# Optimization experiments

Hardware: AMD Instinct MI355X
Metric: run time of the kernel (lower is better)

The kernel has to match this reference:

```python
import jax, jax.numpy as jnp
import numpy as np
import math

B, S, H = 2, 2048, 2048
NH, HD = 16, 128           # num_heads, head_dim; num_kv_heads == num_heads (MHA)
THETA = 10000.0


def setup_inputs() -> dict:
    key = jax.random.key(0)
    ks = jax.random.split(key, 5)
    scale = 0.02
    hidden_states = jax.random.normal(ks[0], (B, S, H), jnp.float32)
    q_w = jax.random.normal(ks[1], (H, H), jnp.float32) * scale
    k_w = jax.random.normal(ks[2], (H, H), jnp.float32) * scale
    v_w = jax.random.normal(ks[3], (H, H), jnp.float32) * scale
    o_w = jax.random.normal(ks[4], (H, H), jnp.float32) * scale
    # additive causal mask, finite large-negative (as HF builds it)
    causal = jnp.tril(jnp.ones((S, S), bool))
    attention_mask = jnp.where(causal, 0.0, -1e9).astype(jnp.float32)[None, None]  # [1,1,S,S]
    position_ids = jnp.broadcast_to(jnp.arange(S, dtype=jnp.int64), (B, S))
    return {
        "hidden_states": hidden_states,
        "q_w": q_w, "k_w": k_w, "v_w": v_w, "o_w": o_w,
        "attention_mask": attention_mask,
        "position_ids": position_ids,
    }


def _rotate_half(x):
    x1, x2 = x[..., : x.shape[-1] // 2], x[..., x.shape[-1] // 2 :]
    return jnp.concatenate((-x2, x1), axis=-1)


def _rope_cos_sin(position_ids):
    inv_freq = 1.0 / (THETA ** (jnp.arange(0, HD, 2, dtype=jnp.float32) / HD))  # [HD/2]
    freqs = position_ids.astype(jnp.float32)[:, :, None] * inv_freq[None, None, :]  # [B,S,HD/2]
    emb = jnp.concatenate((freqs, freqs), axis=-1)  # [B,S,HD]
    # unsqueeze head dim (unsqueeze_dim=1 after transpose to [B,H,S,D])
    return jnp.cos(emb)[:, None], jnp.sin(emb)[:, None]  # [B,1,S,HD]


def reference(hidden_states, q_w, k_w, v_w, o_w, attention_mask, position_ids):
    # projections (torch Linear: y = x @ W^T), split heads -> [B,NH,S,HD]
    def proj(w):
        return jnp.einsum('bsh,oh->bso', hidden_states, w).reshape(B, S, NH, HD).transpose(0, 2, 1, 3)
    q, k, v = proj(q_w), proj(k_w), proj(v_w)

    cos, sin = _rope_cos_sin(position_ids)
    q = q * cos + _rotate_half(q) * sin
    k = k * cos + _rotate_half(k) * sin

    scores = jnp.einsum('bhqd,bhkd->bhqk', q, k) / math.sqrt(HD)  # [B,NH,S,S]
    scores = scores + attention_mask
    attn = jax.nn.softmax(scores, axis=-1)  # dropout p=0.0 -> identity
    out = jnp.einsum('bhqk,bhkd->bhqd', attn, v)  # [B,NH,S,HD]
    out = out.transpose(0, 2, 1, 3).reshape(B, S, H)
    return jnp.einsum('bsh,oh->bso', out, o_w)
```

## Files before the change

kernel.cpp:

```cpp
#include <hip/hip_runtime.h>
#include <hip/hip_bf16.h>

using bf16 = __hip_bfloat16;
typedef short  short8  __attribute__((ext_vector_type(8)));
typedef float  float4_ __attribute__((ext_vector_type(4)));
typedef int    int4_   __attribute__((ext_vector_type(4)));

typedef __attribute__((address_space(1))) const void* gas_ptr;
typedef __attribute__((address_space(3))) void*       las_ptr;

#define MFMA_BF16(a, b, c) __builtin_amdgcn_mfma_f32_16x16x32_bf16((a), (b), (c), 0, 0, 0)

__device__ __forceinline__ float bf2f(bf16 v) { return __bfloat162float(v); }
__device__ __forceinline__ bf16  f2bf(float v) { return __float2bfloat16(v); }

#define BAR() do { asm volatile("" ::: "memory"); __builtin_amdgcn_s_barrier(); asm volatile("" ::: "memory"); } while (0)
#define WAITLGKM0() asm volatile("s_waitcnt lgkmcnt(0)" ::: "memory")

__global__ __launch_bounds__(256)
void cvt_all(const float* __restrict__ X,  const float* __restrict__ Wq,
             const float* __restrict__ Wk, const float* __restrict__ Wv,
             const float* __restrict__ Wo,
             bf16* __restrict__ Xb,  bf16* __restrict__ Wqb,
             bf16* __restrict__ Wkb, bf16* __restrict__ Wvb,
             bf16* __restrict__ Wob)
{
    const size_t i = ((size_t)blockIdx.x * 256 + threadIdx.x) * 8;
    const float* src; bf16* dst; size_t off;
    if (i < 8388608)       { src = X;  dst = Xb;  off = i; }
    else if (i < 12582912) { src = Wq; dst = Wqb; off = i - 8388608; }
    else if (i < 16777216) { src = Wk; dst = Wkb; off = i - 12582912; }
    else if (i < 20971520) { src = Wv; dst = Wvb; off = i - 16777216; }
    else                   { src = Wo; dst = Wob; off = i - 20971520; }
    const float4_ a = *(const float4_*)(src + off);
    const float4_ b = *(const float4_*)(src + off + 4);
    union { short8 s; bf16 h[8]; } u;
#pragma unroll
    for (int j = 0; j < 4; ++j) { u.h[j] = f2bf(a[j]); u.h[j + 4] = f2bf(b[j]); }
    *(short8*)(dst + off) = u.s;
}

__global__ __launch_bounds__(512, 2)
void gemm_bn128(const bf16* __restrict__ Ap, const bf16* __restrict__ Wp,
                bf16* __restrict__ Oq, float* __restrict__ OF, int mode)
{
    constexpr int NT = 32;
    __shared__ bf16 As0[2 * 256 * 64];
    __shared__ bf16 Bs0[2 * 128 * 64];

    const int nwg  = gridDim.x * gridDim.y;
    const int bid0 = blockIdx.y * gridDim.x + blockIdx.x;
    const int cpx  = nwg >> 3;
    const int swzb = (bid0 & 7) * cpx + (bid0 >> 3);
    const int bn = (swzb % gridDim.x) * 128;
    const int bm = (swzb / gridDim.x) * 256;

    const int tid  = threadIdx.x;
    const int w    = tid >> 6;
    const int ln   = tid & 63;
    const int r15  = ln & 15;
    const int quad = ln >> 4;
    const int wr   = w >> 1;
    const int wc   = w & 1;

    const int srow = ln >> 3;
    const int scol = ((ln & 7) ^ srow) * 8;
    const int w8   = w * 8;
    const int cx   = (r15 & 7) * 8;

#define STAGE_A(pb, ts) do {                                                \
    _Pragma("unroll")                                                       \
    for (int c = 0; c < 4; ++c) {                                           \
        const int rl = c * 64 + w8;                                         \
        __builtin_amdgcn_global_load_lds(                                   \
            (gas_ptr)(Ap + (size_t)(bm + rl + srow) * 2048 + (ts) * 64 + scol), \
            (las_ptr)(As0 + (pb) * 16384 + rl * 64), 16, 0, 0);             \
    } } while (0)

#define STAGE_B0(pb, ts) do {                                               \
    const int rl = w8;                                                      \
    __builtin_amdgcn_global_load_lds(                                       \
        (gas_ptr)(Wp + (size_t)(bn + rl + srow) * 2048 + (ts) * 64 + scol), \
        (las_ptr)(Bs0 + (pb) * 8192 + rl * 64), 16, 0, 0);                  \
    } while (0)

#define STAGE_B1(pb, ts) do {                                               \
    const int rl = 64 + w8;                                                 \
    __builtin_amdgcn_global_load_lds(                                       \
        (gas_ptr)(Wp + (size_t)(bn + rl + srow) * 2048 + (ts) * 64 + scol), \
        (las_ptr)(Bs0 + (pb) * 8192 + rl * 64), 16, 0, 0);                  \
    } while (0)

#define LDA() do {                                                          \
    _Pragma("unroll")                                                       \
    for (int mi = 0; mi < 4; ++mi) {                                        \
        const int row = wr * 64 + mi * 16 + r15;                            \
        a[mi][0] = *(const short8*)(As0 + p * 16384 + row * 64 + ((quad * 8) ^ cx));      \
        a[mi][1] = *(const short8*)(As0 + p * 16384 + row * 64 + ((32 + quad * 8) ^ cx)); \
    } } while (0)

#define LDB(qn) do {                                                        \
    _Pragma("unroll")                                                       \
    for (int j = 0; j < 2; ++j) {                                           \
        const int row = wc * 64 + ((qn) * 2 + j) * 16 + r15;                \
        b[j][0] = *(const short8*)(Bs0 + p * 8192 + row * 64 + ((quad * 8) ^ cx));      \
        b[j][1] = *(const short8*)(Bs0 + p * 8192 + row * 64 + ((32 + quad * 8) ^ cx)); \
    } } while (0)

#define MM(qn) do {                                                         \
    __builtin_amdgcn_s_setprio(1);                                          \
    _Pragma("unroll")                                                       \
    for (int mi = 0; mi < 4; ++mi)                                          \
        _Pragma("unroll")                                                   \
        for (int j = 0; j < 2; ++j)                                         \
            _Pragma("unroll")                                               \
            for (int kk = 0; kk < 2; ++kk)                                  \
                acc[mi][(qn) * 2 + j] =                                     \
                    MFMA_BF16(a[mi][kk], b[j][kk], acc[mi][(qn) * 2 + j]);  \
    __builtin_amdgcn_s_setprio(0); } while (0)

    float4_ acc[4][4];
    const float4_ fzero = {0.f, 0.f, 0.f, 0.f};
#pragma unroll
    for (int i = 0; i < 4; ++i)
#pragma unroll
        for (int j = 0; j < 4; ++j) acc[i][j] = fzero;

    short8 a[4][2], b[2][2];

    STAGE_A(0, 0); STAGE_B0(0, 0); STAGE_B1(0, 0);
    STAGE_A(1, 1); STAGE_B0(1, 1);
    asm volatile("s_waitcnt vmcnt(5)" ::: "memory");
    BAR();

    for (int t = 0; t < NT; ++t) {
        const int p = t & 1, pq = p ^ 1;
        LDA(); LDB(0);
        if (t + 1 < NT) STAGE_B1(pq, t + 1);
        asm volatile("s_waitcnt lgkmcnt(8)" ::: "memory");
        BAR(); WAITLGKM0();
        MM(0);
        BAR();
        LDB(1);
        if (t + 2 < NT) { STAGE_A(p, t + 2); STAGE_B0(p, t + 2); }
        BAR(); WAITLGKM0();
        MM(1);
        if (t >= NT - 2) { asm volatile("s_waitcnt vmcnt(0)" ::: "memory"); }
        else             { asm volatile("s_waitcnt vmcnt(5)" ::: "memory"); }
        BAR();
    }

#pragma unroll
    for (int mi = 0; mi < 4; ++mi) {
#pragma unroll
        for (int ni = 0; ni < 4; ++ni) {
#pragma unroll
            for (int r = 0; r < 4; ++r) {
                const int row = bm + wr * 64 + mi * 16 + quad * 4 + r;
                const int col = bn + wc * 64 + ni * 16 + r15;
                const float v = acc[mi][ni][r];
                if (mode == 0) {
                    const int z = col >> 11, c2 = col & 2047;
                    const int h = c2 >> 7, d = c2 & 127;
                    const int bb = row >> 11, s = row & 2047;
                    Oq[(size_t)z * 8388608 + (((size_t)bb * 16 + h) * 2048 + s) * 128 + d] = f2bf(v);
                } else {
                    OF[(size_t)row * 2048 + col] = v;
                }
            }
        }
    }
#undef STAGE_A
#undef STAGE_B0
#undef STAGE_B1
#undef LDA
#undef LDB
#undef MM
}

__global__ __launch_bounds__(256)
void rope_scale(bf16* __restrict__ Q, bf16* __restrict__ Kb)
{
    const int idx = blockIdx.x * 256 + threadIdx.x;
    const int d  = idx & 63;
    const int s  = (idx >> 6) & 2047;
    const int bh = idx >> 17;
    const size_t base = ((size_t)bh * 2048 + s) * 128;

    const float inv_freq = expf(-(float)d * (9.210340371976184f / 64.f));
    const float ang = (float)s * inv_freq;
    const float c = cosf(ang), sn = sinf(ang);
    const float sc = 0.08838834764831845f;

    const float q1 = bf2f(Q[base + d]), q2 = bf2f(Q[base + d + 64]);
    Q[base + d]      = f2bf((q1 * c - q2 * sn) * sc);
    Q[base + d + 64] = f2bf((q2 * c + q1 * sn) * sc);

    const float k1 = bf2f(Kb[base + d]), k2 = bf2f(Kb[base + d + 64]);
    Kb[base + d]      = f2bf(k1 * c - k2 * sn);
    Kb[base + d + 64] = f2bf(k2 * c + k1 * sn);
}

__global__ __launch_bounds__(512)
void flash_attn(const bf16* __restrict__ Qg, const bf16* __restrict__ Kg,
                const bf16* __restrict__ Vg, bf16* __restrict__ Og)
{
    constexpr int S = 2048;
    const int pr = blockIdx.x;
    const int bh = blockIdx.y;
    const int b = bh >> 4, h = bh & 15;
    const size_t base = (size_t)bh * S * 128;
    const bf16* Qp = Qg + base;
    const bf16* Kp = Kg + base;
    const bf16* Vp = Vg + base;

    const int tid  = threadIdx.x;
    const int wave = tid >> 6;
    const int ln   = tid & 63;
    const int r15  = ln & 15;
    const int quad = ln >> 4;
    const int sid  = wave & 3;
    const int hi   = wave >> 2;

    __shared__ bf16 Ks[64][136];
    __shared__ bf16 Vt[128][72];
    __shared__ bf16 Ps[8][32][72];

    const int strip = hi ? (15 - pr) : pr;
    const int qrow0 = strip * 128 + sid * 32;
    const int dt    = qrow0 >> 6;
    const int ktmax = 2 * (15 - pr) + 1;

    short8 qf[2][4];
#pragma unroll
    for (int rf = 0; rf < 2; ++rf)
#pragma unroll
        for (int ks = 0; ks < 4; ++ks)
            qf[rf][ks] = *(const short8*)&Qp[(size_t)(qrow0 + rf * 16 + r15) * 128
                                             + ks * 32 + quad * 8];

    float4_ acc_o[2][8];
    const float4_ fzero = {0.f, 0.f, 0.f, 0.f};
#pragma unroll
    for (int rf = 0; rf < 2; ++rf)
#pragma unroll
        for (int of = 0; of < 8; ++of) acc_o[rf][of] = fzero;
    float m_run[2][4], l_run[2][4];
#pragma unroll
    for (int rf = 0; rf < 2; ++rf)
#pragma unroll
        for (int r = 0; r < 4; ++r) { m_run[rf][r] = -__builtin_inff(); l_run[rf][r] = 0.f; }

    const int kr = tid >> 4;
    const int kc = (tid & 15) * 8;
    const int vd = wave * 16;

    {
#pragma unroll
        for (int p = 0; p < 2; ++p)
            *(int4_*)&Ks[kr + p * 32][kc] =
                *(const int4_*)&Kp[(size_t)(kr + p * 32) * 128 + kc];
        union { int4_ v; bf16 h[8]; } u;
#pragma unroll
        for (int p = 0; p < 2; ++p) {
            u.v = *(const int4_*)&Vp[(size_t)ln * 128 + vd + p * 8];
#pragma unroll
            for (int j = 0; j < 8; ++j)
                Vt[vd + p * 8 + j][ln] = u.h[j];
        }
    }
    __syncthreads();

    for (int kt = 0; kt <= ktmax; ++kt) {
        const bool more = (kt < ktmax);

        int4_ kpre0, kpre1, vpre0, vpre1;
        if (more) {
            const int krow = (kt + 1) * 64;
            kpre0 = *(const int4_*)&Kp[(size_t)(krow + kr) * 128 + kc];
            kpre1 = *(const int4_*)&Kp[(size_t)(krow + kr + 32) * 128 + kc];
            vpre0 = *(const int4_*)&Vp[(size_t)(krow + ln) * 128 + vd];
            vpre1 = *(const int4_*)&Vp[(size_t)(krow + ln) * 128 + vd + 8];
        }

        if (kt <= dt) {
            float4_ sacc[2][4];
            __builtin_amdgcn_s_setprio(1);
#pragma unroll
            for (int nf = 0; nf < 4; ++nf) {
                sacc[0][nf] = fzero;
                sacc[1][nf] = fzero;
#pragma unroll
                for (int ks = 0; ks < 4; ++ks) {
                    short8 kf = *(const short8*)&Ks[nf * 16 + r15][ks * 32 + quad * 8];
                    sacc[0][nf] = MFMA_BF16(qf[0][ks], kf, sacc[0][nf]);
                    sacc[1][nf] = MFMA_BF16(qf[1][ks], kf, sacc[1][nf]);
                }
            }
            __builtin_amdgcn_s_setprio(0);

            if (kt == dt) {
#pragma unroll
                for (int rf = 0; rf < 2; ++rf) {
                    const int ro = (qrow0 & 63) + rf * 16 + quad * 4;
#pragma unroll
                    for (int nf = 0; nf < 4; ++nf) {
                        const int col = nf * 16 + r15;
#pragma unroll
                        for (int r = 0; r < 4; ++r)
                            if (col > ro + r) sacc[rf][nf][r] = -__builtin_inff();
                    }
                }
            }

#pragma unroll
            for (int rf = 0; rf < 2; ++rf) {
                float mnew[4], alpha[4];
#pragma unroll
                for (int r = 0; r < 4; ++r) {
                    float rm = fmaxf(fmaxf(sacc[rf][0][r], sacc[rf][1][r]),
                                     fmaxf(sacc[rf][2][r], sacc[rf][3][r]));
                    rm = fmaxf(rm, __shfl_xor(rm, 1));
                    rm = fmaxf(rm, __shfl_xor(rm, 2));
                    rm = fmaxf(rm, __shfl_xor(rm, 4));
                    rm = fmaxf(rm, __shfl_xor(rm, 8));
                    mnew[r]  = fmaxf(m_run[rf][r], rm);
                    alpha[r] = __expf(m_run[rf][r] - mnew[r]);
                    m_run[rf][r] = mnew[r];
                }
                float rs[4] = {0.f, 0.f, 0.f, 0.f};
#pragma unroll
                for (int nf = 0; nf < 4; ++nf) {
#pragma unroll
                    for (int r = 0; r < 4; ++r) {
                        const float pp = __expf(sacc[rf][nf][r] - mnew[r]);
                        rs[r] += pp;
                        Ps[wave][rf * 16 + quad * 4 + r][nf * 16 + r15] = f2bf(pp);
                    }
                }
#pragma unroll
                for (int r = 0; r < 4; ++r) {
                    float t = rs[r];
                    t += __shfl_xor(t, 1);
                    t += __shfl_xor(t, 2);
                    t += __shfl_xor(t, 4);
                    t += __shfl_xor(t, 8);
                    l_run[rf][r] = l_run[rf][r] * alpha[r] + t;
                }
#pragma unroll
                for (int of = 0; of < 8; ++of)
#pragma unroll
                    for (int r = 0; r < 4; ++r)
                        acc_o[rf][of][r] *= alpha[r];
            }

            __builtin_amdgcn_s_setprio(1);
#pragma unroll
            for (int k2 = 0; k2 < 2; ++k2) {
                short8 pf0 = *(const short8*)&Ps[wave][r15][k2 * 32 + quad * 8];
                short8 pf1 = *(const short8*)&Ps[wave][16 + r15][k2 * 32 + quad * 8];
#pragma unroll
                for (int of = 0; of < 8; ++of) {
                    short8 vf = *(const short8*)&Vt[of * 16 + r15][k2 * 32 + quad * 8];
                    acc_o[0][of] = MFMA_BF16(pf0, vf, acc_o[0][of]);
                    acc_o[1][of] = MFMA_BF16(pf1, vf, acc_o[1][of]);
                }
            }
            __builtin_amdgcn_s_setprio(0);
        }

        __syncthreads();
        if (more) {
            *(int4_*)&Ks[kr][kc]      = kpre0;
            *(int4_*)&Ks[kr + 32][kc] = kpre1;
            union { int4_ v; bf16 h[8]; } u;
            u.v = vpre0;
#pragma unroll
            for (int j = 0; j < 8; ++j) Vt[vd + j][ln] = u.h[j];
            u.v = vpre1;
#pragma unroll
            for (int j = 0; j < 8; ++j) Vt[vd + 8 + j][ln] = u.h[j];
        }
        __syncthreads();
    }

#pragma unroll
    for (int rf = 0; rf < 2; ++rf) {
#pragma unroll
        for (int r = 0; r < 4; ++r) {
            const float inv = 1.f / l_run[rf][r];
            const int  s  = qrow0 + rf * 16 + quad * 4 + r;
            const size_t ob = (((size_t)b * S + s) * 16 + h) * 128;
#pragma unroll
            for (int of = 0; of < 8; ++of)
                Og[ob + of * 16 + r15] = f2bf(acc_o[rf][of][r] * inv);
        }
    }
}

extern "C" void kernel_launch(void* const* d_in, const int* in_sizes, int n_in,
                              void* d_out, int out_size, void* d_ws, size_t ws_size,
                              hipStream_t stream)
{
    const float* X  = (const float*)d_in[0];
    const float* Wq = (const float*)d_in[1];
    const float* Wk = (const float*)d_in[2];
    const float* Wv = (const float*)d_in[3];
    const float* Wo = (const float*)d_in[4];
    float* out = (float*)d_out;

    bf16* Xb  = (bf16*)d_ws;
    bf16* Wqb = Xb  + 8388608;
    bf16* Wkb = Wqb + 4194304;
    bf16* Wvb = Wkb + 4194304;
    bf16* Wob = Wvb + 4194304;
    bf16* q   = Wob + 4194304;
    bf16* k   = q   + 8388608;
    bf16* v   = k   + 8388608;
    bf16* ao  = v   + 8388608;

    dim3 blk(256);
    cvt_all<<<dim3(12288), blk, 0, stream>>>(X, Wq, Wk, Wv, Wo,
                                             Xb, Wqb, Wkb, Wvb, Wob);
    gemm_bn128<<<dim3(48, 16), dim3(512), 0, stream>>>(Xb, Wqb, q, nullptr, 0);
    rope_scale<<<dim3((2 * 16 * 2048 * 64) / 256), blk, 0, stream>>>(q, k);
    flash_attn<<<dim3(8, 32), dim3(512), 0, stream>>>(q, k, v, ao);
    gemm_bn128<<<dim3(16, 16), dim3(512), 0, stream>>>(ao, Wob, nullptr, out, 1);
}
```

Baseline: 440.1 us.

## Use DPP row reductions and lazy softmax rescaling in attention

Replaces the shfl_xor-based 16-lane max/sum reductions with DPP lane-permute intrinsics, avoiding LDS-routed shuffles. Also adds a wave-uniform lazy rescale: the running max is updated and the output accumulator and row sum are rescaled only when the new block max exceeds the running max by more than a threshold. This skips most exp and multiply work on acc_o. The risk is that unnormalised exponentials can grow up to e^8, which bf16 P and fp32 accumulators should tolerate but which slightly changes numerics.

New measurement: 421.7 us. 4.2% less time.

```diff
diff --git a/kernel.cpp b/kernel.cpp
--- a/kernel.cpp
+++ b/kernel.cpp
@@ -16,6 +16,26 @@
 
 #define BAR() do { asm volatile("" ::: "memory"); __builtin_amdgcn_s_barrier(); asm volatile("" ::: "memory"); } while (0)
 #define WAITLGKM0() asm volatile("s_waitcnt lgkmcnt(0)" ::: "memory")
+
+template<int CTRL>
+__device__ __forceinline__ float dppmv(float x) {
+    return __int_as_float(__builtin_amdgcn_update_dpp(
+        0, __float_as_int(x), CTRL, 0xF, 0xF, true));
+}
+__device__ __forceinline__ float row16_max(float x) {
+    x = fmaxf(x, dppmv<0xB1>(x));
+    x = fmaxf(x, dppmv<0x4E>(x));
+    x = fmaxf(x, dppmv<0x124>(x));
+    x = fmaxf(x, dppmv<0x128>(x));
+    return x;
+}
+__device__ __forceinline__ float row16_sum(float x) {
+    x += dppmv<0xB1>(x);
+    x += dppmv<0x4E>(x);
+    x += dppmv<0x124>(x);
+    x += dppmv<0x128>(x);
+    return x;
+}
 
 __global__ __launch_bounds__(256)
 void cvt_all(const float* __restrict__ X,  const float* __restrict__ Wq,
@@ -315,18 +335,27 @@
 
 #pragma unroll
             for (int rf = 0; rf < 2; ++rf) {
-                float mnew[4], alpha[4];
+                float rm4[4];
+                float g = 0.f;
 #pragma unroll
                 for (int r = 0; r < 4; ++r) {
                     float rm = fmaxf(fmaxf(sacc[rf][0][r], sacc[rf][1][r]),
                                      fmaxf(sacc[rf][2][r], sacc[rf][3][r]));
-                    rm = fmaxf(rm, __shfl_xor(rm, 1));
-                    rm = fmaxf(rm, __shfl_xor(rm, 2));
-                    rm = fmaxf(rm, __shfl_xor(rm, 4));
-                    rm = fmaxf(rm, __shfl_xor(rm, 8));
-                    mnew[r]  = fmaxf(m_run[rf][r], rm);
-                    alpha[r] = __expf(m_run[rf][r] - mnew[r]);
-                    m_run[rf][r] = mnew[r];
+                    rm4[r] = row16_max(rm);
+                    g = fmaxf(g, rm4[r] - m_run[rf][r]);
+                }
+                const bool resc = !__all(g <= 8.f);
+                float mnew[4], alpha[4];
+                if (resc) {
+#pragma unroll
+                    for (int r = 0; r < 4; ++r) {
+                        mnew[r]  = fmaxf(m_run[rf][r], rm4[r]);
+                        alpha[r] = __expf(m_run[rf][r] - mnew[r]);
+                        m_run[rf][r] = mnew[r];
+                    }
+                } else {
+#pragma unroll
+                    for (int r = 0; r < 4; ++r) { mnew[r] = m_run[rf][r]; alpha[r] = 1.f; }
                 }
                 float rs[4] = {0.f, 0.f, 0.f, 0.f};
 #pragma unroll
@@ -340,18 +369,17 @@
                 }
 #pragma unroll
                 for (int r = 0; r < 4; ++r) {
-                    float t = rs[r];
-                    t += __shfl_xor(t, 1);
-                    t += __shfl_xor(t, 2);
-                    t += __shfl_xor(t, 4);
-                    t += __shfl_xor(t, 8);
-                    l_run[rf][r] = l_run[rf][r] * alpha[r] + t;
-                }
-#pragma unroll
-                for (int of = 0; of < 8; ++of)
-#pragma unroll
-                    for (int r = 0; r < 4; ++r)
-                        acc_o[rf][of][r] *= alpha[r];
+                    const float t = row16_sum(rs[r]);
+                    l_run[rf][r] = resc ? (l_run[rf][r] * alpha[r] + t)
+                                        : (l_run[rf][r] + t);
+                }
+                if (resc) {
+#pragma unroll
+                    for (int of = 0; of < 8; ++of)
+#pragma unroll
+                        for (int r = 0; r < 4; ++r)
+                            acc_o[rf][of][r] *= alpha[r];
+                }
             }
 
             __builtin_amdgcn_s_setprio(1);
```
